# Optimization experiments

Hardware: AMD Instinct MI355X
Metric: run time of the kernel (lower is better)

The kernel has to match this reference:

```python
import jax, jax.numpy as jnp
import numpy as np

N_NODES = 100000
N_EDGES = 1600000
IN_DIM, HID_DIM, OUT_DIM = 128, 128, 64


def _sage_conv(x, src, dst, W_l, W_r, b, num_nodes):
    # messages: gather source-node features, mean-aggregate at destination
    msgs = x[src]                                            # [E, D]
    agg = jax.ops.segment_sum(msgs, dst, num_segments=num_nodes)   # [N, D]
    deg = jax.ops.segment_sum(jnp.ones((src.shape[0],), x.dtype), dst,
                              num_segments=num_nodes)        # [N]
    mean = jnp.where(deg[:, None] > 0, agg / jnp.maximum(deg, 1.0)[:, None], 0.0)
    # PyG SAGEConv: lin_l(aggr) + lin_r(root); bias lives in lin_l
    return mean @ W_l + b + x @ W_r


def setup_inputs() -> dict:
    key = jax.random.key(0)
    ks = jax.random.split(key, 8)
    x = jax.random.normal(ks[0], (N_NODES, IN_DIM), dtype=jnp.float32)
    edge_index = jax.random.randint(ks[1], (2, N_EDGES), 0, N_NODES, dtype=jnp.int64)
    s1 = 1.0 / np.sqrt(IN_DIM)
    s2 = 1.0 / np.sqrt(HID_DIM)
    return {
        "x": x,
        "edge_index": edge_index,
        "W1_l": jax.random.normal(ks[2], (IN_DIM, HID_DIM), jnp.float32) * s1,
        "W1_r": jax.random.normal(ks[3], (IN_DIM, HID_DIM), jnp.float32) * s1,
        "b1": jnp.zeros((HID_DIM,), jnp.float32),
        "W2_l": jax.random.normal(ks[4], (HID_DIM, OUT_DIM), jnp.float32) * s2,
        "W2_r": jax.random.normal(ks[5], (HID_DIM, OUT_DIM), jnp.float32) * s2,
        "b2": jnp.zeros((OUT_DIM,), jnp.float32),
    }


def reference(x, edge_index, W1_l, W1_r, b1, W2_l, W2_r, b2):
    src, dst = edge_index[0], edge_index[1]  # source_to_target flow
    h = _sage_conv(x, src, dst, W1_l, W1_r, b1, N_NODES)
    h = jax.nn.relu(h)
    # dropout is identity in eval mode
    h = _sage_conv(h, src, dst, W2_l, W2_r, b2, N_NODES)
    return h
```

## Files before the change

kernel.cpp:

```cpp
#include <hip/hip_runtime.h>

#define N_NODES 100000
#define N_EDGES 1600000
#define IN_DIM 128
#define HID_DIM 128
#define OUT_DIM 64

#define BKT_SHIFT 8
#define NPB 256
#define NBKT ((N_NODES + NPB - 1) / NPB)
#define BKT_CAP 5120
#define BIN_CHUNK 4096

#define CC_CSR NBKT
#define CC_CONV (N_NODES / 4)
#define CC_WT 192

typedef __attribute__((ext_vector_type(8))) short short8;
typedef __attribute__((ext_vector_type(4))) float f32x4;
typedef __attribute__((ext_vector_type(2))) short s16x2;

__device__ __forceinline__ float bf2f(unsigned short h) {
    unsigned int u = ((unsigned int)h) << 16;
    return __builtin_bit_cast(float, u);
}
__device__ __forceinline__ unsigned short f2bf(float f) {
    unsigned int u = __builtin_bit_cast(unsigned int, f);
    u += 0x7FFFu + ((u >> 16) & 1u);
    return (unsigned short)(u >> 16);
}

#define XSCALE 21.166666f
#define XINV   0.047244094f
#define ZQ     10.583333f
#define ZINV   0.094488189f

__device__ __forceinline__ void acc_i8x4(unsigned v, s16x2& L, s16x2& H) {
    s16x2 sv = __builtin_bit_cast(s16x2, v);
    H += sv >> 8;
    L += (s16x2)(sv << 8) >> 8;
}

__device__ __forceinline__ int wswz(int m, int k, int KW) {
    return (m * KW + k) ^ ((m & 7) << 3);
}

__global__ __launch_bounds__(256) void bin_kernel(
        const int* __restrict__ src, const int* __restrict__ dst,
        int* __restrict__ cursor, unsigned* __restrict__ binned) {
    __shared__ int cnt[NBKT];
    __shared__ int sbase[NBKT];
    const int b = blockIdx.x, t = threadIdx.x;
    for (int i = t; i < NBKT; i += 256) cnt[i] = 0;
    __syncthreads();
    const int e0 = b * BIN_CHUNK;
    unsigned val[16];
    int bkt[16], rank[16];
    #pragma unroll
    for (int k = 0; k < 16; ++k) {
        int e = e0 + k * 256 + t;
        if (e < N_EDGES) {
            int d = dst[e];
            bkt[k] = d >> BKT_SHIFT;
            val[k] = (unsigned)src[e] | ((unsigned)(d & (NPB - 1)) << 17);
            rank[k] = atomicAdd(&cnt[bkt[k]], 1);
        } else {
            bkt[k] = -1;
        }
    }
    __syncthreads();
    for (int i = t; i < NBKT; i += 256)
        sbase[i] = cnt[i] ? atomicAdd(&cursor[i], cnt[i]) : 0;
    __syncthreads();
    #pragma unroll
    for (int k = 0; k < 16; ++k)
        if (bkt[k] >= 0)
            binned[(size_t)bkt[k] * BKT_CAP + sbase[bkt[k]] + rank[k]] = val[k];
}

__global__ __launch_bounds__(256) void csr_conv_kernel(
        const unsigned* __restrict__ binned, const int* __restrict__ cursor,
        int* __restrict__ offsets, int* __restrict__ csr_src,
        const float* __restrict__ x, unsigned short* __restrict__ xh,
        unsigned char* __restrict__ xq,
        const float* __restrict__ W1l, const float* __restrict__ W1r,
        const float* __restrict__ W2l, const float* __restrict__ W2r,
        unsigned short* __restrict__ WT1, unsigned short* __restrict__ WT2T) {
    int b = blockIdx.x;
    const int t = threadIdx.x;

    if (b < CC_CSR) {
        __shared__ int deg[NPB];
        __shared__ int cur[NPB];
        __shared__ int wsums[4];
        __shared__ int sbase_sh;
        const int lane = t & 63, wid = t >> 6;

        int ps = 0;
        for (int i = t; i < b; i += 256) ps += cursor[i];
        #pragma unroll
        for (int off = 32; off; off >>= 1) ps += __shfl_down(ps, off, 64);
        if (lane == 0) wsums[wid] = ps;
        deg[t] = 0;
        __syncthreads();
        if (t == 0) sbase_sh = wsums[0] + wsums[1] + wsums[2] + wsums[3];
        __syncthreads();
        const int base = sbase_sh;
        const int n0 = b << BKT_SHIFT;
        const int cnt = cursor[b];
        const unsigned* __restrict__ ebase = binned + (size_t)b * BKT_CAP;

        for (int i = t; i < cnt; i += 256)
            atomicAdd(&deg[ebase[i] >> 17], 1);
        __syncthreads();

        int d = deg[t];
        int s = d;
        #pragma unroll
        for (int off = 1; off < 64; off <<= 1) {
            int u = __shfl_up(s, off, 64);
            if (lane >= off) s += u;
        }
        if (lane == 63) wsums[wid] = s;
        __syncthreads();
        int add = 0;
        for (int w = 0; w < wid; ++w) add += wsums[w];
        const int excl = s + add - d;
        cur[t] = excl;
        const int n = n0 + t;
        if (n <= N_NODES) offsets[n] = base + excl;
        __syncthreads();

        for (int i = t; i < cnt; i += 256) {
            unsigned v = ebase[i];
            int pos = atomicAdd(&cur[v >> 17], 1);
            csr_src[base + pos] = (int)(v & 0x1FFFFu);
        }
        return;
    }

    b -= CC_CSR;
    if (b < CC_CONV) {
        const int w = t >> 6, lane = t & 63;
        const int row = b * 4 + w;
        float2 v = *(const float2*)(x + (size_t)row * 128 + lane * 2);
        unsigned pk = (unsigned)f2bf(v.x) | ((unsigned)f2bf(v.y) << 16);
        *(unsigned*)(xh + (size_t)row * 128 + lane * 2) = pk;
        int q0 = (int)__float2int_rn(fminf(fmaxf(v.x * XSCALE, -127.f), 127.f));
        int q1 = (int)__float2int_rn(fminf(fmaxf(v.y * XSCALE, -127.f), 127.f));
        *(unsigned short*)(xq + (size_t)row * 128 + lane * 2) =
            (unsigned short)((q0 & 0xFF) | ((q1 & 0xFF) << 8));
        return;
    }

    int i = (b - CC_CONV) * 256 + t;
    if (i < 128 * 256) {
        int m = i >> 8, k = i & 255;
        float v = (k < 128) ? W1l[(size_t)k * 128 + m] : W1r[(size_t)(k - 128) * 128 + m];
        WT1[wswz(m, k, 256)] = f2bf(v);
        return;
    }
    i -= 128 * 256;
    if (i < 128 * 128) {
        int j = i >> 7, k = i & 127;
        float v = (j < 64) ? W2l[(size_t)k * 64 + j] : W2r[(size_t)k * 64 + (j - 64)];
        WT2T[wswz(j, k, 128)] = f2bf(v);
    }
}

__global__ __launch_bounds__(256) void agg1_int8(
        const unsigned char* __restrict__ xq, const int* __restrict__ offsets,
        const int* __restrict__ csr_src, unsigned short* __restrict__ mh) {
    const int wv = threadIdx.x >> 6;
    const int lane = threadIdx.x & 63;
    const int slot = lane >> 3, dp = lane & 7;
    const int node = (blockIdx.x * 4 + wv) * 8 + slot;
    const int beg = offsets[node];
    const int deg = offsets[node + 1] - beg;

    s16x2 aL[4], aH[4];
    #pragma unroll
    for (int i = 0; i < 4; ++i) { aL[i] = (s16x2)0; aH[i] = (s16x2)0; }

    for (int c = 0; c < deg; c += 8) {
        int my = beg + c + dp;
        int idx8 = csr_src[my < beg + deg ? my : beg];
        #pragma unroll
        for (int jj = 0; jj < 8; ++jj) {
            if (c + jj < deg) {
                int s = __shfl(idx8, slot * 8 + jj, 64);
                uint4 v = *(const uint4*)(xq + (size_t)s * 128 + dp * 16);
                acc_i8x4(v.x, aL[0], aH[0]);
                acc_i8x4(v.y, aL[1], aH[1]);
                acc_i8x4(v.z, aL[2], aH[2]);
                acc_i8x4(v.w, aL[3], aH[3]);
            }
        }
    }

    const float inv = (deg > 0) ? XINV / (float)deg : 0.0f;
    unsigned w[8];
    #pragma unroll
    for (int d = 0; d < 4; ++d) {
        w[2 * d]     = (unsigned)f2bf((float)aL[d].x * inv)
                     | ((unsigned)f2bf((float)aH[d].x * inv) << 16);
        w[2 * d + 1] = (unsigned)f2bf((float)aL[d].y * inv)
                     | ((unsigned)f2bf((float)aH[d].y * inv) << 16);
    }
    uint4* o = (uint4*)(mh + (size_t)node * 128 + dp * 16);
    o[0] = make_uint4(w[0], w[1], w[2], w[3]);
    o[1] = make_uint4(w[4], w[5], w[6], w[7]);
}

__global__ __launch_bounds__(256) void gemm12_kernel(
        const unsigned short* __restrict__ mh, const unsigned short* __restrict__ xh,
        const unsigned short* __restrict__ WT1, const unsigned short* __restrict__ WT2T,
        const float* __restrict__ b1, const float* __restrict__ b2,
        unsigned char* __restrict__ zq, unsigned short* __restrict__ pout) {
    __shared__ unsigned short Ws1[128 * 256];
    __shared__ unsigned short Ws2[128 * 128];
    __shared__ unsigned short hT[128][136];
    const int t = threadIdx.x;
    {
        const uint4* s1 = (const uint4*)WT1;
        uint4* d1 = (uint4*)Ws1;
        #pragma unroll
        for (int r = 0; r < 16; ++r) d1[t + r * 256] = s1[t + r * 256];
        const uint4* s2 = (const uint4*)WT2T;
        uint4* d2 = (uint4*)Ws2;
        #pragma unroll
        for (int r = 0; r < 8; ++r) d2[t + r * 256] = s2[t + r * 256];
    }
    const int wave = t >> 6;
    const int lane = t & 63;
    const int rowbase = blockIdx.x * 128 + wave * 32;
    const int lrow = lane & 15;
    const int kq = (lane >> 4) * 8;
    const int rsw = (lrow & 7) << 3;
    const int colq = lane & 15;
    const int rowq = (lane >> 4) * 4;

    f32x4 acc[2][8];
    #pragma unroll
    for (int rt = 0; rt < 2; ++rt)
        #pragma unroll
        for (int ct = 0; ct < 8; ++ct) acc[rt][ct] = (f32x4)0.f;

    int r0 = rowbase + lrow;      if (r0 > N_NODES - 1) r0 = N_NODES - 1;
    int r1 = rowbase + 16 + lrow; if (r1 > N_NODES - 1) r1 = N_NODES - 1;

    __syncthreads();

    #pragma unroll
    for (int half = 0; half < 2; ++half) {
        const unsigned short* __restrict__ A = half ? xh : mh;
        #pragma unroll
        for (int kc = 0; kc < 4; ++kc) {
            const int kofs = kc * 32 + kq;
            short8 a0 = *(const short8*)(A + (size_t)r0 * 128 + kofs);
            short8 a1 = *(const short8*)(A + (size_t)r1 * 128 + kofs);
            #pragma unroll
            for (int ct = 0; ct < 8; ++ct) {
                short8 bb = *(const short8*)&Ws1[(((ct * 16 + lrow) << 8)
                                                  + (half << 7) + kofs) ^ rsw];
                acc[0][ct] = __builtin_amdgcn_mfma_f32_16x16x32_bf16(a0, bb, acc[0][ct], 0, 0, 0);
                acc[1][ct] = __builtin_amdgcn_mfma_f32_16x16x32_bf16(a1, bb, acc[1][ct], 0, 0, 0);
            }
        }
    }

    #pragma unroll
    for (int ct = 0; ct < 8; ++ct) {
        const int col = ct * 16 + colq;
        const float bc = b1[col];
        #pragma unroll
        for (int rt = 0; rt < 2; ++rt) {
            #pragma unroll
            for (int i = 0; i < 4; ++i) {
                const int rl = wave * 32 + rt * 16 + rowq + i;
                hT[rl][col] = f2bf(fmaxf(acc[rt][ct][i] + bc, 0.f));
            }
        }
    }

    #pragma unroll
    for (int rt = 0; rt < 2; ++rt)
        #pragma unroll
        for (int ct = 0; ct < 8; ++ct) acc[rt][ct] = (f32x4)0.f;

    #pragma unroll
    for (int kc = 0; kc < 4; ++kc) {
        const int kofs = kc * 32 + kq;
        short8 a0 = *(const short8*)&hT[wave * 32 + lrow][kofs];
        short8 a1 = *(const short8*)&hT[wave * 32 + 16 + lrow][kofs];
        #pragma unroll
        for (int ct = 0; ct < 8; ++ct) {
            short8 bb = *(const short8*)&Ws2[(((ct * 16 + lrow) << 7) + kofs) ^ rsw];
            acc[0][ct] = __builtin_amdgcn_mfma_f32_16x16x32_bf16(a0, bb, acc[0][ct], 0, 0, 0);
            acc[1][ct] = __builtin_amdgcn_mfma_f32_16x16x32_bf16(a1, bb, acc[1][ct], 0, 0, 0);
        }
    }

    #pragma unroll
    for (int rt = 0; rt < 2; ++rt) {
        #pragma unroll
        for (int i = 0; i < 4; ++i) {
            const int row = rowbase + rt * 16 + rowq + i;
            if (row < N_NODES) {
                unsigned char* zr = zq + (size_t)row * 64 + colq;
                #pragma unroll
                for (int ct = 0; ct < 4; ++ct) {
                    float v = fminf(fmaxf(acc[rt][ct][i] * ZQ, -127.f), 127.f);
                    zr[ct * 16] = (unsigned char)(signed char)__float2int_rn(v);
                }
            }
        }
    }
    #pragma unroll
    for (int ct = 4; ct < 8; ++ct) {
        const int col = ct * 16 + colq;
        const float bc = b2[col - 64];
        #pragma unroll
        for (int rt = 0; rt < 2; ++rt) {
            #pragma unroll
            for (int i = 0; i < 4; ++i) {
                const int row = rowbase + rt * 16 + rowq + i;
                if (row < N_NODES)
                    pout[(size_t)row * 64 + (col - 64)] = f2bf(acc[rt][ct][i] + bc);
            }
        }
    }
}

__global__ __launch_bounds__(256) void agg2_out_kernel(
        const unsigned char* __restrict__ zq, const unsigned short* __restrict__ pout,
        const int* __restrict__ offsets, const int* __restrict__ csr_src,
        float* __restrict__ out) {
    const int wv = threadIdx.x >> 6;
    const int lane = threadIdx.x & 63;
    const int slot = lane >> 3, dp = lane & 7;
    const int node = (blockIdx.x * 4 + wv) * 8 + slot;
    const int beg = offsets[node];
    const int deg = offsets[node + 1] - beg;

    s16x2 aL[2], aH[2];
    #pragma unroll
    for (int i = 0; i < 2; ++i) { aL[i] = (s16x2)0; aH[i] = (s16x2)0; }

    for (int c = 0; c < deg; c += 8) {
        int my = beg + c + dp;
        int idx8 = csr_src[my < beg + deg ? my : beg];
        #pragma unroll
        for (int jj = 0; jj < 8; ++jj) {
            if (c + jj < deg) {
                int s = __shfl(idx8, slot * 8 + jj, 64);
                uint2 v = *(const uint2*)(zq + (size_t)s * 64 + dp * 8);
                acc_i8x4(v.x, aL[0], aH[0]);
                acc_i8x4(v.y, aL[1], aH[1]);
            }
        }
    }

    const float inv = (deg > 0) ? ZINV / (float)deg : 0.0f;
    const unsigned short* pp = pout + (size_t)node * 64 + dp * 8;
    float* oo = out + (size_t)node * 64 + dp * 8;
    #pragma unroll
    for (int d = 0; d < 2; ++d) {
        ushort4 p = *(const ushort4*)(pp + d * 4);
        float4 o;
        o.x = (float)aL[d].x * inv + bf2f(p.x);
        o.y = (float)aH[d].x * inv + bf2f(p.y);
        o.z = (float)aL[d].y * inv + bf2f(p.z);
        o.w = (float)aH[d].y * inv + bf2f(p.w);
        *(float4*)(oo + d * 4) = o;
    }
}


extern "C" void kernel_launch(void* const* d_in, const int* in_sizes, int n_in,
                              void* d_out, int out_size, void* d_ws, size_t ws_size,
                              hipStream_t stream) {
    const float* x   = (const float*)d_in[0];
    const int*   ei  = (const int*)d_in[1];
    const float* W1l = (const float*)d_in[2];
    const float* W1r = (const float*)d_in[3];
    const float* b1  = (const float*)d_in[4];
    const float* W2l = (const float*)d_in[5];
    const float* W2r = (const float*)d_in[6];
    const float* b2  = (const float*)d_in[7];
    float* out = (float*)d_out;

    const int* src = ei;
    const int* dst = ei + N_EDGES;

    char* ws = (char*)d_ws;
    int* cursor   = (int*)ws;
    int* offsets  = cursor + 512;
    int* csr_src  = offsets + N_NODES + 16;
    unsigned char*  xq  = (unsigned char*)(csr_src + N_EDGES + 64);
    unsigned short* xh  = (unsigned short*)(xq + (size_t)N_NODES * 128);
    unsigned short* mh  = xh + (size_t)N_NODES * 128;
    unsigned char*  zq  = (unsigned char*)(mh + (size_t)N_NODES * 128);
    unsigned short* pout = (unsigned short*)(zq + (size_t)N_NODES * 64);
    unsigned short* WT1  = pout + (size_t)N_NODES * 64;
    unsigned short* WT2T = WT1 + 128 * 256;
    unsigned* binned = (unsigned*)mh;

    hipMemsetAsync(cursor, 0, NBKT * sizeof(int), stream);

    bin_kernel<<<(N_EDGES + BIN_CHUNK - 1) / BIN_CHUNK, 256, 0, stream>>>(
        src, dst, cursor, binned);

    csr_conv_kernel<<<CC_CSR + CC_CONV + CC_WT, 256, 0, stream>>>(
        binned, cursor, offsets, csr_src, x, xh, xq,
        W1l, W1r, W2l, W2r, WT1, WT2T);

    agg1_int8<<<N_NODES / 32, 256, 0, stream>>>(xq, offsets, csr_src, mh);

    gemm12_kernel<<<(N_NODES + 127) / 128, 256, 0, stream>>>(
        mh, xh, WT1, WT2T, b1, b2, zq, pout);

    agg2_out_kernel<<<N_NODES / 32, 256, 0, stream>>>(zq, pout, offsets, csr_src, out);
}
```

Baseline: 186.9 us.

## Split int8 feature tables into column chunks to shrink gather working set

The int8 node feature tables xq and zq are stored as two column halves, each a contiguous plane of 64 or 32 bytes per node. The aggregation kernels now handle one half per block (block parity selects the chunk), so each half-table is smaller and more likely to stay in L2/LLC during the random neighbor gathers. The cost is that edge indices and offsets are read twice, one pass per chunk, and thread-to-node mappings change to 4 or 2 lanes per node with bounds guards.

```diff
diff --git a/kernel.cpp b/kernel.cpp
--- a/kernel.cpp
+++ b/kernel.cpp
@@ -148,7 +148,9 @@
         *(unsigned*)(xh + (size_t)row * 128 + lane * 2) = pk;
         int q0 = (int)__float2int_rn(fminf(fmaxf(v.x * XSCALE, -127.f), 127.f));
         int q1 = (int)__float2int_rn(fminf(fmaxf(v.y * XSCALE, -127.f), 127.f));
-        *(unsigned short*)(xq + (size_t)row * 128 + lane * 2) =
+        const int ch = lane >> 5;
+        const int off = (lane & 31) * 2;
+        *(unsigned short*)(xq + ((size_t)ch * N_NODES + row) * 64 + off) =
             (unsigned short)((q0 & 0xFF) | ((q1 & 0xFF) << 8));
         return;
     }
@@ -171,25 +173,30 @@
 __global__ __launch_bounds__(256) void agg1_int8(
         const unsigned char* __restrict__ xq, const int* __restrict__ offsets,
         const int* __restrict__ csr_src, unsigned short* __restrict__ mh) {
+    const int chunk = blockIdx.x & 1;
+    const int bb = blockIdx.x >> 1;
     const int wv = threadIdx.x >> 6;
     const int lane = threadIdx.x & 63;
-    const int slot = lane >> 3, dp = lane & 7;
-    const int node = (blockIdx.x * 4 + wv) * 8 + slot;
-    const int beg = offsets[node];
-    const int deg = offsets[node + 1] - beg;
+    const int slot = lane >> 2, dp = lane & 3;
+    const int node = (bb * 4 + wv) * 16 + slot;
+    const bool valid = node < N_NODES;
+    const int nd = valid ? node : N_NODES - 1;
+    const int beg = offsets[nd];
+    const int deg = offsets[nd + 1] - beg;
+    const unsigned char* __restrict__ xc = xq + (size_t)chunk * N_NODES * 64;
 
     s16x2 aL[4], aH[4];
     #pragma unroll
     for (int i = 0; i < 4; ++i) { aL[i] = (s16x2)0; aH[i] = (s16x2)0; }
 
-    for (int c = 0; c < deg; c += 8) {
+    for (int c = 0; c < deg; c += 4) {
         int my = beg + c + dp;
-        int idx8 = csr_src[my < beg + deg ? my : beg];
-        #pragma unroll
-        for (int jj = 0; jj < 8; ++jj) {
+        int idx4 = csr_src[my < beg + deg ? my : beg];
+        #pragma unroll
+        for (int jj = 0; jj < 4; ++jj) {
             if (c + jj < deg) {
-                int s = __shfl(idx8, slot * 8 + jj, 64);
-                uint4 v = *(const uint4*)(xq + (size_t)s * 128 + dp * 16);
+                int s = __shfl(idx4, slot * 4 + jj, 64);
+                uint4 v = *(const uint4*)(xc + (size_t)s * 64 + dp * 16);
                 acc_i8x4(v.x, aL[0], aH[0]);
                 acc_i8x4(v.y, aL[1], aH[1]);
                 acc_i8x4(v.z, aL[2], aH[2]);
@@ -198,18 +205,20 @@
         }
     }
 
-    const float inv = (deg > 0) ? XINV / (float)deg : 0.0f;
-    unsigned w[8];
-    #pragma unroll
-    for (int d = 0; d < 4; ++d) {
-        w[2 * d]     = (unsigned)f2bf((float)aL[d].x * inv)
-                     | ((unsigned)f2bf((float)aH[d].x * inv) << 16);
-        w[2 * d + 1] = (unsigned)f2bf((float)aL[d].y * inv)
-                     | ((unsigned)f2bf((float)aH[d].y * inv) << 16);
-    }
-    uint4* o = (uint4*)(mh + (size_t)node * 128 + dp * 16);
-    o[0] = make_uint4(w[0], w[1], w[2], w[3]);
-    o[1] = make_uint4(w[4], w[5], w[6], w[7]);
+    if (valid) {
+        const float inv = (deg > 0) ? XINV / (float)deg : 0.0f;
+        unsigned w[8];
+        #pragma unroll
+        for (int d = 0; d < 4; ++d) {
+            w[2 * d]     = (unsigned)f2bf((float)aL[d].x * inv)
+                         | ((unsigned)f2bf((float)aH[d].x * inv) << 16);
+            w[2 * d + 1] = (unsigned)f2bf((float)aL[d].y * inv)
+                         | ((unsigned)f2bf((float)aH[d].y * inv) << 16);
+        }
+        uint4* o = (uint4*)(mh + (size_t)node * 128 + chunk * 64 + dp * 16);
+        o[0] = make_uint4(w[0], w[1], w[2], w[3]);
+        o[1] = make_uint4(w[4], w[5], w[6], w[7]);
+    }
 }
 
 __global__ __launch_bounds__(256) void gemm12_kernel(
@@ -307,11 +316,11 @@
         for (int i = 0; i < 4; ++i) {
             const int row = rowbase + rt * 16 + rowq + i;
             if (row < N_NODES) {
-                unsigned char* zr = zq + (size_t)row * 64 + colq;
                 #pragma unroll
                 for (int ct = 0; ct < 4; ++ct) {
                     float v = fminf(fmaxf(acc[rt][ct][i] * ZQ, -127.f), 127.f);
-                    zr[ct * 16] = (unsigned char)(signed char)__float2int_rn(v);
+                    zq[((size_t)(ct >> 1) * N_NODES + row) * 32 + (ct & 1) * 16 + colq] =
+                        (unsigned char)(signed char)__float2int_rn(v);
                 }
             }
         }
@@ -336,43 +345,53 @@
         const unsigned char* __restrict__ zq, const unsigned short* __restrict__ pout,
         const int* __restrict__ offsets, const int* __restrict__ csr_src,
         float* __restrict__ out) {
+    const int chunk = blockIdx.x & 1;
+    const int bb = blockIdx.x >> 1;
     const int wv = threadIdx.x >> 6;
     const int lane = threadIdx.x & 63;
-    const int slot = lane >> 3, dp = lane & 7;
-    const int node = (blockIdx.x * 4 + wv) * 8 + slot;
-    const int beg = offsets[node];
-    const int deg = offsets[node + 1] - beg;
-
-    s16x2 aL[2], aH[2];
-    #pragma unroll
-    for (int i = 0; i < 2; ++i) { aL[i] = (s16x2)0; aH[i] = (s16x2)0; }
-
-    for (int c = 0; c < deg; c += 8) {
+    const int slot = lane >> 1, dp = lane & 1;
+    const int node = (bb * 4 + wv) * 32 + slot;
+    const bool valid = node < N_NODES;
+    const int nd = valid ? node : N_NODES - 1;
+    const int beg = offsets[nd];
+    const int deg = offsets[nd + 1] - beg;
+    const unsigned char* __restrict__ zc = zq + (size_t)chunk * N_NODES * 32;
+
+    s16x2 aL[4], aH[4];
+    #pragma unroll
+    for (int i = 0; i < 4; ++i) { aL[i] = (s16x2)0; aH[i] = (s16x2)0; }
+
+    for (int c = 0; c < deg; c += 2) {
         int my = beg + c + dp;
-        int idx8 = csr_src[my < beg + deg ? my : beg];
-        #pragma unroll
-        for (int jj = 0; jj < 8; ++jj) {
+        int idx2 = csr_src[my < beg + deg ? my : beg];
+        #pragma unroll
+        for (int jj = 0; jj < 2; ++jj) {
             if (c + jj < deg) {
-                int s = __shfl(idx8, slot * 8 + jj, 64);
-                uint2 v = *(const uint2*)(zq + (size_t)s * 64 + dp * 8);
+                int s = __shfl(idx2, slot * 2 + jj, 64);
+                uint4 v = *(const uint4*)(zc + (size_t)s * 32 + dp * 16);
                 acc_i8x4(v.x, aL[0], aH[0]);
                 acc_i8x4(v.y, aL[1], aH[1]);
-            }
-        }
-    }
-
-    const float inv = (deg > 0) ? ZINV / (float)deg : 0.0f;
-    const unsigned short* pp = pout + (size_t)node * 64 + dp * 8;
-    float* oo = out + (size_t)node * 64 + dp * 8;
-    #pragma unroll
-    for (int d = 0; d < 2; ++d) {
-        ushort4 p = *(const ushort4*)(pp + d * 4);
-        float4 o;
-        o.x = (float)aL[d].x * inv + bf2f(p.x);
-        o.y = (float)aH[d].x * inv + bf2f(p.y);
-        o.z = (float)aL[d].y * inv + bf2f(p.z);
-        o.w = (float)aH[d].y * inv + bf2f(p.w);
-        *(float4*)(oo + d * 4) = o;
+                acc_i8x4(v.z, aL[2], aH[2]);
+                acc_i8x4(v.w, aL[3], aH[3]);
+            }
+        }
+    }
+
+    if (valid) {
+        const float inv = (deg > 0) ? ZINV / (float)deg : 0.0f;
+        const int dbase = chunk * 32 + dp * 16;
+        const unsigned short* pp = pout + (size_t)node * 64 + dbase;
+        float* oo = out + (size_t)node * 64 + dbase;
+        #pragma unroll
+        for (int d = 0; d < 4; ++d) {
+            ushort4 p = *(const ushort4*)(pp + d * 4);
+            float4 o;
+            o.x = (float)aL[d].x * inv + bf2f(p.x);
+            o.y = (float)aH[d].x * inv + bf2f(p.y);
+            o.z = (float)aL[d].y * inv + bf2f(p.z);
+            o.w = (float)aH[d].y * inv + bf2f(p.w);
+            *(float4*)(oo + d * 4) = o;
+        }
     }
 }
 
@@ -415,10 +434,12 @@
         binned, cursor, offsets, csr_src, x, xh, xq,
         W1l, W1r, W2l, W2r, WT1, WT2T);
 
-    agg1_int8<<<N_NODES / 32, 256, 0, stream>>>(xq, offsets, csr_src, mh);
+    const int a1b = ((N_NODES + 63) / 64) * 2;
+    agg1_int8<<<a1b, 256, 0, stream>>>(xq, offsets, csr_src, mh);
 
     gemm12_kernel<<<(N_NODES + 127) / 128, 256, 0, stream>>>(
         mh, xh, WT1, WT2T, b1, b2, zq, pout);
 
-    agg2_out_kernel<<<N_NODES / 32, 256, 0, stream>>>(zq, pout, offsets, csr_src, out);
-}
+    const int a2b = ((N_NODES + 127) / 128) * 2;
+    agg2_out_kernel<<<a2b, 256, 0, stream>>>(zq, pout, offsets, csr_src, out);
+}
```

After: 190.6 us. No clear change (+2.0%).
